# Kernel optimization log

Measured on AMD Instinct MI355X. Metric: run time of the kernel, lower is better.

The kernel has to match this reference:

```python
import jax, jax.numpy as jnp
import numpy as np

NUM_HEADS = 12
LN_EPS = 1e-5
SM_EPS = 1e-6


def layer_norm(x, w, b):
    m = x.mean(-1, keepdims=True)
    v = ((x - m) ** 2).mean(-1, keepdims=True)
    return (x - m) / jnp.sqrt(v + LN_EPS) * w + b


def softmax_with_policy(attn, policy):
    # attn: [B,H,N,N], policy: [B,N,1]
    B, H, N, _ = attn.shape
    attn_policy = policy.reshape(B, 1, 1, N)
    eye = jnp.eye(N, dtype=attn.dtype)[None, None]
    attn_policy = attn_policy + (1.0 - attn_policy) * eye
    m = attn.max(axis=-1, keepdims=True)
    e = jnp.exp(attn - m) * attn_policy
    return (e + SM_EPS / N) / (e.sum(axis=-1, keepdims=True) + SM_EPS)


def create_ys(ncdf, n_ref):
    # ncdf: [B, N-1]; returns ys: [B, n_ref-1]
    B = ncdf.shape[0]
    ys = jnp.linspace(0.0, 1.0, n_ref - 1, dtype=ncdf.dtype)[None, :]
    ys_start = jnp.min(ncdf + (ncdf == 0).astype(ncdf.dtype) * 1e8, axis=1, keepdims=True)
    steps = jnp.arange(n_ref - 1, dtype=ncdf.dtype)[None, :]
    return ys_start + (ys * (n_ref - 2) - ys_start * steps) / (n_ref - 2)


def get_unique_indices(indices, max_value):
    # duplicate indices are replaced by max_value, then re-sorted
    B = indices.shape[0]
    s = jnp.sort(indices, axis=1)
    shifted = jnp.concatenate([s[:, 1:], jnp.ones((B, 1), s.dtype)], axis=1)
    uniq = jnp.where(shifted == s, max_value, s)
    return jnp.sort(uniq, axis=1)


def ats_block(x, policy, norm1_w, norm1_b, qkv_w, proj_w, proj_b,
              norm2_w, norm2_b, fc1_w, fc1_b, fc2_w, fc2_b,
              n_tokens, n_ref_tokens):
    B, N, C = x.shape
    H = NUM_HEADS
    dh = C // H
    scale = dh ** -0.5

    xn = layer_norm(x, norm1_w, norm1_b)
    qkv = (xn @ qkv_w).reshape(B, N, 3, H, dh).transpose(2, 0, 3, 1, 4)  # [3,B,H,N,dh]
    qkv = qkv * policy[None, :, None, :, :]
    q, k, v = qkv[0], qkv[1], qkv[2]

    attn = softmax_with_policy(jnp.einsum('bhnd,bhmd->bhnm', q, k) * scale, policy)

    # --- score assignment ---
    v_norm = jnp.linalg.norm(v.transpose(0, 2, 1, 3).reshape(B, N, C), axis=2)  # [B,N]
    sig = attn[:, :, 0, :].sum(axis=1) * v_norm      # CLS attention row summed over heads
    sig = sig[:, 1:]
    sig = sig / sig.sum(axis=1, keepdims=True)
    order = jnp.argsort(sig, axis=1)                 # ascending
    sorted_scores = jnp.take_along_axis(sig, order, axis=1)

    # --- inverse transform sampling ---
    cdf = jnp.cumsum(sorted_scores, axis=1)
    cmin = cdf.min(axis=1, keepdims=True)
    cmax = cdf.max(axis=1, keepdims=True)
    ncdf = (cdf - cmin) / (cmax - cmin)              # [B, N-1]
    ys = create_ys(ncdf, n_ref_tokens)               # [B, n_ref-1]
    diff = (n_ref_tokens - 1) - (N - 1)
    ncdf_p = jnp.pad(ncdf, ((0, 0), (diff, 0))) if diff > 0 else ncdf
    tokens_to_pick = jnp.argmin(jnp.abs(ys[:, :, None] - ncdf_p[:, None, :]), axis=2) - diff

    uniq = get_unique_indices(tokens_to_pick, N - 1)[:, :N - 1]
    ui = uniq[:, :n_tokens - 1]                      # [B, n_tokens-1]

    # reorder attn rows / raw tokens by significance order, pad a zero row at N-1
    oidx = jnp.broadcast_to(order[:, None, :, None], (B, H, N - 1, N))
    attn_sorted = jnp.take_along_axis(attn[:, :, 1:, :], oidx, axis=2)
    attn_tmp = jnp.pad(attn_sorted, ((0, 0), (0, 0), (0, 1), (0, 0)))
    rx_sorted = jnp.take_along_axis(x[:, 1:, :], jnp.broadcast_to(order[:, :, None], (B, N - 1, C)), axis=1)
    rx_tmp = jnp.pad(rx_sorted, ((0, 0), (0, 1), (0, 0)))

    uidx = jnp.broadcast_to(ui[:, None, :, None], (B, H, n_tokens - 1, N))
    attn_sel = jnp.take_along_axis(attn_tmp, uidx, axis=2)
    rx_sel = jnp.take_along_axis(rx_tmp, jnp.broadcast_to(ui[:, :, None], (B, n_tokens - 1, C)), axis=1)

    attn_new = jnp.concatenate([attn[:, :, 0:1, :], attn_sel], axis=2)     # [B,H,n_tokens,N]
    selected_x = jnp.concatenate([x[:, 0:1, :], rx_sel], axis=1)           # [B,n_tokens,C]
    pol_new = (ui != N - 1).astype(x.dtype)[:, :, None]
    pol_new = jnp.pad(pol_new, ((0, 0), (1, 0), (0, 0)), constant_values=1.0)  # [B,n_tokens,1]

    out = jnp.einsum('bhnm,bhmd->bhnd', attn_new, v)
    out = out.transpose(0, 2, 1, 3).reshape(B, n_tokens, C)
    out = (out @ proj_w + proj_b) * pol_new

    x2 = selected_x + out
    h = jax.nn.gelu(layer_norm(x2, norm2_w, norm2_b) @ fc1_w + fc1_b, approximate=False)
    x2 = x2 + (h @ fc2_w + fc2_b) * pol_new
    return x2, pol_new


def setup_inputs() -> dict:
    key = jax.random.key(0)
    ks = jax.random.split(key, 6)
    B, N, C = 8, 785, 768
    init = lambda k, sh, fan: jax.random.normal(k, sh, jnp.float32) * (fan ** -0.5)
    return {
        'x': jax.random.normal(ks[0], (B, N, C), jnp.float32),
        'policy': jnp.ones((B, N, 1), jnp.float32),
        'norm1_w': jnp.ones((C,), jnp.float32),
        'norm1_b': jnp.zeros((C,), jnp.float32),
        'qkv_w': init(ks[1], (C, 3 * C), C),
        'proj_w': init(ks[2], (C, C), C),
        'proj_b': jnp.zeros((C,), jnp.float32),
        'norm2_w': jnp.ones((C,), jnp.float32),
        'norm2_b': jnp.zeros((C,), jnp.float32),
        'fc1_w': init(ks[3], (C, 4 * C), C),
        'fc1_b': jnp.zeros((4 * C,), jnp.float32),
        'fc2_w': init(ks[4], (4 * C, C), 4 * C),
        'fc2_b': jnp.zeros((C,), jnp.float32),
        'n_tokens': 393,
        'n_ref_tokens': 785,
    }


def reference(x, policy, norm1_w, norm1_b, qkv_w, proj_w, proj_b,
              norm2_w, norm2_b, fc1_w, fc1_b, fc2_w, fc2_b,
              n_tokens, n_ref_tokens):
    return ats_block(x, policy, norm1_w, norm1_b, qkv_w, proj_w, proj_b,
                     norm2_w, norm2_b, fc1_w, fc1_b, fc2_w, fc2_b,
                     int(n_tokens), int(n_ref_tokens))
```

## Files before the change

### kernel.cpp

```cpp
#include <hip/hip_runtime.h>
#include <hip/hip_bf16.h>
#include <float.h>
#include <math.h>
#include <stdint.h>

constexpr int B_   = 8;
constexpr int N_   = 785;
constexpr int C_   = 768;
constexpr int H_   = 12;
constexpr int DH_  = 64;
constexpr int NT_  = 393;
constexpr int QKVC = 3 * C_;
constexpr int BN   = B_ * N_;
constexpr int BT   = B_ * NT_;
constexpr int MSEL = N_ - 1;
constexpr float  SCALE_F = 0.125f;
constexpr double LNEPS   = 1e-5;
constexpr double SMEPS   = 1e-6;

#define DEV static __device__ __forceinline__

typedef __hip_bfloat16 bf16;
typedef __attribute__((ext_vector_type(8))) short frag8;
typedef __attribute__((ext_vector_type(4))) float facc4;

DEV short f2b(float v) { return (short)__hip_bfloat16_raw(__float2bfloat16(v)).x; }
DEV float b2f(short s) {
  union { unsigned int u; float f; } cv;
  cv.u = ((unsigned int)(unsigned short)s) << 16;
  return cv.f;
}

DEV double blockReduceSumD(double v, double* scratch, int nw) {
#pragma unroll
  for (int o = 32; o; o >>= 1) v += __shfl_xor(v, o);
  int lane = threadIdx.x & 63, wid = threadIdx.x >> 6;
  __syncthreads();
  if (lane == 0) scratch[wid] = v;
  __syncthreads();
  double r = scratch[0];
  for (int i = 1; i < nw; i++) r += scratch[i];
  return r;
}
DEV double blockReduceMaxD(double v, double* scratch, int nw) {
#pragma unroll
  for (int o = 32; o; o >>= 1) v = fmax(v, __shfl_xor(v, o));
  int lane = threadIdx.x & 63, wid = threadIdx.x >> 6;
  __syncthreads();
  if (lane == 0) scratch[wid] = v;
  __syncthreads();
  double r = scratch[0];
  for (int i = 1; i < nw; i++) r = fmax(r, scratch[i]);
  return r;
}
DEV float blockReduceSumF(float v, float* scratch, int nw) {
#pragma unroll
  for (int o = 32; o; o >>= 1) v += __shfl_xor(v, o);
  int lane = threadIdx.x & 63, wid = threadIdx.x >> 6;
  __syncthreads();
  if (lane == 0) scratch[wid] = v;
  __syncthreads();
  float r = scratch[0];
  for (int i = 1; i < nw; i++) r += scratch[i];
  return r;
}
DEV float blockReduceMaxF(float v, float* scratch, int nw) {
#pragma unroll
  for (int o = 32; o; o >>= 1) v = fmaxf(v, __shfl_xor(v, o));
  int lane = threadIdx.x & 63, wid = threadIdx.x >> 6;
  __syncthreads();
  if (lane == 0) scratch[wid] = v;
  __syncthreads();
  float r = scratch[0];
  for (int i = 1; i < nw; i++) r = fmaxf(r, scratch[i]);
  return r;
}

__global__ __launch_bounds__(256) void ln1_kernel(
    const float* __restrict__ x, const float* __restrict__ w, const float* __restrict__ b,
    double* __restrict__ xn64, bf16* __restrict__ xnb) {
  int row = blockIdx.x;
  int t = threadIdx.x;
  __shared__ double scr[8];
  const float* xr = x + (size_t)row * C_;
  double vals[3];
#pragma unroll
  for (int i = 0; i < 3; i++) vals[i] = (double)xr[t + i * 256];
  double s = vals[0] + vals[1] + vals[2];
  s = blockReduceSumD(s, scr, 4);
  double mean = s / (double)C_;
  double vs = 0.0;
#pragma unroll
  for (int i = 0; i < 3; i++) { double d = vals[i] - mean; vs += d * d; }
  vs = blockReduceSumD(vs, scr, 4);
  double inv = 1.0 / sqrt(vs / (double)C_ + LNEPS);
#pragma unroll
  for (int i = 0; i < 3; i++) {
    int c = t + i * 256;
    double o = (vals[i] - mean) * inv * (double)w[c] + (double)b[c];
    xn64[(size_t)row * C_ + c] = o;
    xnb[(size_t)row * C_ + c] = __float2bfloat16((float)o);
  }
}

__global__ __launch_bounds__(256) void transpose_bf16(
    const float* __restrict__ W, bf16* __restrict__ Wt, int K, int N) {
  __shared__ float tile[32][33];
  int k0 = blockIdx.y * 32, n0 = blockIdx.x * 32;
  int tx = threadIdx.x & 31, ty = threadIdx.x >> 5;
  for (int i = ty; i < 32; i += 8) {
    int k = k0 + i, n = n0 + tx;
    tile[i][tx] = (k < K && n < N) ? W[(size_t)k * N + n] : 0.f;
  }
  __syncthreads();
  for (int i = ty; i < 32; i += 8) {
    int n = n0 + i, k = k0 + tx;
    if (n < N && k < K) Wt[(size_t)n * K + k] = __float2bfloat16(tile[tx][i]);
  }
}

__global__ __launch_bounds__(256) void gemm_bf16(
    const bf16* __restrict__ A, const bf16* __restrict__ Bt,
    float* __restrict__ Cc, const float* __restrict__ bias,
    const float* __restrict__ rowscale, int M, int K, int Ncols) {
  __shared__ short As[64][40];
  __shared__ short Bs[64][40];
  const short* Ap = (const short*)A;
  const short* Bp = (const short*)Bt;
  int t = threadIdx.x;
  int n0 = blockIdx.x * 64;
  int m0 = blockIdx.y * 64;
  int w = t >> 6, l = t & 63;
  int srow = t >> 2;
  int koff = (t & 3) * 8;
  facc4 acc[4] = {{0, 0, 0, 0}, {0, 0, 0, 0}, {0, 0, 0, 0}, {0, 0, 0, 0}};
  int frow = (l & 15);
  int fk = (l >> 4) * 8;
  for (int k0 = 0; k0 < K; k0 += 32) {
    {
      int4 av = make_int4(0, 0, 0, 0);
      if (m0 + srow < M)
        av = *(const int4*)(Ap + (size_t)(m0 + srow) * K + k0 + koff);
      *(int4*)(&As[srow][koff]) = av;
      int4 bv = *(const int4*)(Bp + (size_t)(n0 + srow) * K + k0 + koff);
      *(int4*)(&Bs[srow][koff]) = bv;
    }
    __syncthreads();
    frag8 a = *(frag8*)(&As[w * 16 + frow][fk]);
#pragma unroll
    for (int nt = 0; nt < 4; nt++) {
      frag8 bfr = *(frag8*)(&Bs[nt * 16 + frow][fk]);
      acc[nt] = __builtin_amdgcn_mfma_f32_16x16x32_bf16(a, bfr, acc[nt], 0, 0, 0);
    }
    __syncthreads();
  }
#pragma unroll
  for (int nt = 0; nt < 4; nt++) {
#pragma unroll
    for (int reg = 0; reg < 4; reg++) {
      int row = m0 + w * 16 + (l >> 4) * 4 + reg;
      int col = n0 + nt * 16 + (l & 15);
      if (row < M) {
        float v = acc[nt][reg];
        if (bias) v += bias[col];
        if (rowscale) v *= rowscale[row];
        Cc[(size_t)row * Ncols + col] = v;
      }
    }
  }
}

__global__ __launch_bounds__(256) void q0_kernel(
    const double* __restrict__ xn64, const float* __restrict__ qkvw,
    const float* __restrict__ policy, double* __restrict__ q064) {
  int b = blockIdx.x;
  int jc = blockIdx.y;
  int t = threadIdx.x;
  int jl = t & 63, ks = t >> 6;
  __shared__ double x0[C_];
  __shared__ double part[4][64];
  for (int i = t; i < C_; i += 256) x0[i] = xn64[(size_t)(b * N_) * C_ + i];
  __syncthreads();
  int j = jc * 64 + jl;
  const float* wp = qkvw + j;
  double a = 0.0;
  int c0 = ks * 192;
#pragma unroll 8
  for (int c = c0; c < c0 + 192; c++) a += x0[c] * (double)wp[(size_t)c * QKVC];
  part[ks][jl] = a;
  __syncthreads();
  if (t < 64) {
    double pol = (double)policy[b * N_];
    q064[b * C_ + jc * 64 + t] =
        (part[0][t] + part[1][t] + part[2][t] + part[3][t]) * pol;
  }
}

__global__ __launch_bounds__(256) void g_kernel(
    const double* __restrict__ q064, const float* __restrict__ qkvw,
    double* __restrict__ g64) {
  int bh = blockIdx.x;
  int b = bh / H_, h = bh % H_;
  int t = threadIdx.x;
  __shared__ double qh[DH_];
  if (t < DH_) qh[t] = q064[b * C_ + h * DH_ + t];
  __syncthreads();
  for (int c = t; c < C_; c += 256) {
    const float* wp = qkvw + (size_t)c * QKVC + C_ + h * DH_;
    double a = 0.0;
#pragma unroll 8
    for (int d = 0; d < DH_; d++) a += qh[d] * (double)wp[d];
    g64[(size_t)bh * C_ + c] = a;
  }
}

__global__ __launch_bounds__(256) void logits_kernel(
    const double* __restrict__ xn64, const double* __restrict__ g64,
    const float* __restrict__ policy, double* __restrict__ l64) {
  int row = blockIdx.x;
  int b = row / N_;
  int n = row % N_;
  int t = threadIdx.x;
  int w = t >> 6, lane = t & 63;
  __shared__ double xr[C_];
  for (int i = t; i < C_; i += 256) xr[i] = xn64[(size_t)row * C_ + i];
  __syncthreads();
  double pol = (double)policy[row];
#pragma unroll
  for (int hh = 0; hh < 3; hh++) {
    int h = w + hh * 4;
    const double* gp = g64 + (size_t)(b * H_ + h) * C_;
    double p = 0.0;
#pragma unroll 4
    for (int i = lane; i < C_; i += 64) p += xr[i] * gp[i];
#pragma unroll
    for (int o = 32; o; o >>= 1) p += __shfl_xor(p, o);
    if (lane == 0) l64[(size_t)(b * H_ + h) * N_ + n] = 0.125 * pol * p;
  }
}

__global__ __launch_bounds__(256) void vnorm_kernel(
    const double* __restrict__ xn64, const float* __restrict__ qkvw,
    const float* __restrict__ policy, double* __restrict__ vnorm2) {
  __shared__ double scr[8];
  int r0 = blockIdx.x * 8;
  int t = threadIdx.x;
  double acc[8][3] = {};
  const double* xb = xn64 + (size_t)r0 * C_;
  for (int c = 0; c < C_; c += 2) {
    const float* wp0 = qkvw + (size_t)c * QKVC + 2 * C_;
    const float* wp1 = wp0 + QKVC;
    double w00 = (double)wp0[t], w01 = (double)wp0[t + 256], w02 = (double)wp0[t + 512];
    double w10 = (double)wp1[t], w11 = (double)wp1[t + 256], w12 = (double)wp1[t + 512];
#pragma unroll
    for (int r = 0; r < 8; r++) {
      double x0 = xb[(size_t)r * C_ + c];
      double x1 = xb[(size_t)r * C_ + c + 1];
      acc[r][0] += x0 * w00; acc[r][1] += x0 * w01; acc[r][2] += x0 * w02;
      acc[r][0] += x1 * w10; acc[r][1] += x1 * w11; acc[r][2] += x1 * w12;
    }
  }
#pragma unroll
  for (int r = 0; r < 8; r++) {
    double p = acc[r][0] * acc[r][0] + acc[r][1] * acc[r][1] + acc[r][2] * acc[r][2];
    double s = blockReduceSumD(p, scr, 4);
    if (t == 0) {
      double pol = (double)policy[r0 + r];
      vnorm2[r0 + r] = s * pol * pol;
    }
  }
}

__global__ __launch_bounds__(256) void softmax0_kernel(
    double* __restrict__ l64, const float* __restrict__ policy) {
  int bh = blockIdx.x;
  int b = bh / H_;
  double* lp = l64 + (size_t)bh * N_;
  __shared__ double scr[8];
  int t = threadIdx.x;
  double mx = -1e300;
  for (int n = t; n < N_; n += 256) mx = fmax(mx, lp[n]);
  mx = blockReduceMaxD(mx, scr, 4);
  double ssum = 0.0;
  for (int n = t; n < N_; n += 256) {
    double pol = (double)policy[b * N_ + n];
    double w = (n == 0) ? 1.0 : pol;
    double e = exp(lp[n] - mx) * w;
    lp[n] = e;
    ssum += e;
  }
  ssum = blockReduceSumD(ssum, scr, 4);
  double denom = ssum + SMEPS;
  double addc = SMEPS / (double)N_;
  for (int n = t; n < N_; n += 256) lp[n] = (lp[n] + addc) / denom;
}

__global__ __launch_bounds__(1024) void select_kernel(
    const double* __restrict__ p0, const double* __restrict__ vnorm2,
    int* __restrict__ selidx, float* __restrict__ poln, float* __restrict__ out_pol) {
  int b = blockIdx.x;
  int t = threadIdx.x;
  __shared__ double sigv[MSEL];
  __shared__ double svals[MSEL];
  __shared__ double nc[MSEL];
  __shared__ int    ord[MSEL];
  __shared__ int    pick[MSEL];
  __shared__ int    spick[MSEL];
  __shared__ int    uq[MSEL];
  __shared__ int    suq[MSEL];
  __shared__ double sh_ys;

  if (t < MSEL) {
    int n = t + 1;
    double s = 0.0;
#pragma unroll
    for (int h = 0; h < H_; h++) s += p0[(size_t)(b * H_ + h) * N_ + n];
    sigv[t] = s * sqrt(vnorm2[b * N_ + n]);
  }
  __syncthreads();
  if (t < MSEL) {
    double v = sigv[t];
    int rank = 0;
    for (int i = 0; i < MSEL; i++) {
      double vi = sigv[i];
      rank += (vi < v) || (vi == v && i < t);
    }
    ord[rank] = t;
    svals[rank] = v;
  }
  __syncthreads();
  if (t == 0) {
    double a = 0.0;
    for (int i = 0; i < MSEL; i++) { a += svals[i]; svals[i] = a; }
  }
  __syncthreads();
  {
    double c0 = svals[0], cN = svals[MSEL - 1];
    if (t < MSEL) nc[t] = (svals[t] - c0) / (cN - c0);
  }
  __syncthreads();
  if (t == 0) {
    double m = 1e300;
    for (int i = 0; i < MSEL; i++) {
      double v = nc[i];
      if (v == 0.0) v += 100000000.0;
      m = fmin(m, v);
    }
    sh_ys = m;
  }
  __syncthreads();
  if (t < MSEL) {
    double s = sh_ys;
    double ysj = (t == MSEL - 1) ? 1.0 : (double)t / 783.0;
    double y = s + (ysj * 783.0 - s * (double)t) / 783.0;
    double bd = 1e300;
    int bi = 0;
    for (int i = 0; i < MSEL; i++) {
      double d = fabs(y - nc[i]);
      if (d < bd) { bd = d; bi = i; }
    }
    pick[t] = bi;
  }
  __syncthreads();
  if (t < MSEL) {
    int p = pick[t];
    int rank = 0;
    for (int i = 0; i < MSEL; i++) {
      int pi = pick[i];
      rank += (pi < p) || (pi == p && i < t);
    }
    spick[rank] = p;
  }
  __syncthreads();
  if (t < MSEL) {
    int s = spick[t];
    int nxt = (t < MSEL - 1) ? spick[t + 1] : 1;
    uq[t] = (nxt == s) ? MSEL : s;
  }
  __syncthreads();
  if (t < MSEL) {
    int u = uq[t];
    int rank = 0;
    for (int i = 0; i < MSEL; i++) {
      int ui = uq[i];
      rank += (ui < u) || (ui == u && i < t);
    }
    suq[rank] = u;
  }
  __syncthreads();
  if (t < NT_) {
    int sel, polI;
    if (t == 0) { sel = 0; polI = 1; }
    else {
      int ut = suq[t - 1];
      polI = (ut != MSEL) ? 1 : 0;
      sel = polI ? (ord[ut] + 1) : -1;
    }
    selidx[b * NT_ + t] = sel;
    poln[b * NT_ + t] = (float)polI;
    out_pol[b * NT_ + t] = (float)polI;
  }
}

__global__ __launch_bounds__(256) void flash_kernel(
    const float* __restrict__ qkv, const int* __restrict__ selidx,
    const float* __restrict__ policy, bf16* __restrict__ attn_bf) {
  int bh = blockIdx.y;
  int b = bh / H_, h = bh % H_;
  int j0 = blockIdx.x * 64;
  int t = threadIdx.x;
  int w = t >> 6, l = t & 63;
  __shared__ short Qs[64][72];
  __shared__ short Ks[64][72];
  __shared__ short Ps[64][72];
  __shared__ short Vs[64][72];
  __shared__ float pol_s[64];
  __shared__ float Vsum[64];

  {
    int jr = t >> 2, d0 = (t & 3) * 16;
    int j = j0 + jr;
    int r = (j < NT_) ? selidx[b * NT_ + j] : -1;
    if (r < 0) r = 0;
    const float* qp = qkv + (size_t)(b * N_ + r) * QKVC + h * DH_ + d0;
#pragma unroll
    for (int i = 0; i < 16; i++) Qs[jr][d0 + i] = f2b(qp[i]);
  }
  if (t < 64) Vsum[t] = 0.f;

  int frow = l & 15, fk = (l >> 4) * 8;
  int base_r = w * 16 + (l >> 4) * 4;
  int coln = l & 15;

  int rrow[4];
#pragma unroll
  for (int r = 0; r < 4; r++) {
    int j = j0 + base_r + r;
    rrow[r] = (j < NT_) ? selidx[b * NT_ + j] : -1;
  }
  float m_run[4] = {-1e30f, -1e30f, -1e30f, -1e30f};
  float s_run[4] = {0.f, 0.f, 0.f, 0.f};
  facc4 Oacc[4] = {{0, 0, 0, 0}, {0, 0, 0, 0}, {0, 0, 0, 0}, {0, 0, 0, 0}};

  for (int n0 = 0; n0 < 832; n0 += 64) {
    {
      int nr = t >> 2, d0 = (t & 3) * 16;
      int n = n0 + nr;
      bool ok = n < N_;
      const float* kp = qkv + (size_t)(b * N_ + (ok ? n : 0)) * QKVC + C_ + h * DH_ + d0;
#pragma unroll
      for (int i = 0; i < 16; i++) Ks[nr][d0 + i] = f2b(ok ? kp[i] : 0.f);
    }
    if (t < 64) {
      int n = n0 + t;
      pol_s[t] = (n < N_) ? policy[b * N_ + n] : 0.f;
    }
    __syncthreads();

    facc4 Sacc[4] = {{0, 0, 0, 0}, {0, 0, 0, 0}, {0, 0, 0, 0}, {0, 0, 0, 0}};
#pragma unroll
    for (int k0 = 0; k0 < 64; k0 += 32) {
      frag8 a = *(frag8*)(&Qs[w * 16 + frow][k0 + fk]);
#pragma unroll
      for (int nt = 0; nt < 4; nt++) {
        frag8 bb = *(frag8*)(&Ks[nt * 16 + frow][k0 + fk]);
        Sacc[nt] = __builtin_amdgcn_mfma_f32_16x16x32_bf16(a, bb, Sacc[nt], 0, 0, 0);
      }
    }
    float S[4][4];
    float tmax[4] = {-1e30f, -1e30f, -1e30f, -1e30f};
#pragma unroll
    for (int nt = 0; nt < 4; nt++) {
#pragma unroll
      for (int r = 0; r < 4; r++) {
        int n = n0 + nt * 16 + coln;
        float v = (n < N_) ? Sacc[nt][r] * SCALE_F : -1e30f;
        S[nt][r] = v;
        tmax[r] = fmaxf(tmax[r], v);
      }
    }
#pragma unroll
    for (int o = 1; o < 16; o <<= 1) {
#pragma unroll
      for (int r = 0; r < 4; r++) tmax[r] = fmaxf(tmax[r], __shfl_xor(tmax[r], o));
    }
    float m_new[4], scl[4], psum[4];
#pragma unroll
    for (int r = 0; r < 4; r++) {
      m_new[r] = fmaxf(m_run[r], tmax[r]);
      scl[r] = expf(m_run[r] - m_new[r]);
      psum[r] = 0.f;
    }
#pragma unroll
    for (int nt = 0; nt < 4; nt++) {
      float pol = pol_s[nt * 16 + coln];
      int n = n0 + nt * 16 + coln;
#pragma unroll
      for (int r = 0; r < 4; r++) {
        float wgt = (n == rrow[r]) ? 1.f : pol;
        float e = expf(S[nt][r] - m_new[r]) * wgt;
        S[nt][r] = e;
        psum[r] += e;
      }
    }
#pragma unroll
    for (int o = 1; o < 16; o <<= 1) {
#pragma unroll
      for (int r = 0; r < 4; r++) psum[r] += __shfl_xor(psum[r], o);
    }
#pragma unroll
    for (int r = 0; r < 4; r++) {
      s_run[r] = s_run[r] * scl[r] + psum[r];
      m_run[r] = m_new[r];
    }
    __syncthreads();

#pragma unroll
    for (int nt = 0; nt < 4; nt++) {
#pragma unroll
      for (int r = 0; r < 4; r++) Ps[base_r + r][nt * 16 + coln] = f2b(S[nt][r]);
    }
    {
      int nr = t >> 2, d0 = (t & 3) * 16;
      int n = n0 + nr;
      bool ok = n < N_;
      const float* vp = qkv + (size_t)(b * N_ + (ok ? n : 0)) * QKVC + 2 * C_ + h * DH_ + d0;
#pragma unroll
      for (int i = 0; i < 16; i++) Vs[d0 + i][nr] = f2b(ok ? vp[i] : 0.f);
    }
    __syncthreads();

    if (t < 64) {
      float a = 0.f;
#pragma unroll 16
      for (int k = 0; k < 64; k++) a += b2f(Vs[t][k]);
      Vsum[t] += a;
    }
#pragma unroll
    for (int dt = 0; dt < 4; dt++) {
#pragma unroll
      for (int r = 0; r < 4; r++) Oacc[dt][r] *= scl[r];
    }
#pragma unroll
    for (int k0 = 0; k0 < 64; k0 += 32) {
      frag8 a = *(frag8*)(&Ps[w * 16 + frow][k0 + fk]);
#pragma unroll
      for (int dt = 0; dt < 4; dt++) {
        frag8 bb = *(frag8*)(&Vs[dt * 16 + frow][k0 + fk]);
        Oacc[dt] = __builtin_amdgcn_mfma_f32_16x16x32_bf16(a, bb, Oacc[dt], 0, 0, 0);
      }
    }
  }
  __syncthreads();
  float addc = 1e-6f / (float)N_;
#pragma unroll
  for (int r = 0; r < 4; r++) {
    int j = j0 + base_r + r;
    if (j >= NT_) continue;
    float denom = s_run[r] + 1e-6f;
#pragma unroll
    for (int dt = 0; dt < 4; dt++) {
      int d = dt * 16 + coln;
      float val = (Oacc[dt][r] + addc * Vsum[d]) / denom;
      attn_bf[(size_t)(b * NT_ + j) * C_ + h * DH_ + d] = __float2bfloat16(val);
    }
  }
}

__global__ __launch_bounds__(256) void e2_kernel(
    const float* __restrict__ cbuf, const float* __restrict__ poln,
    const int* __restrict__ selidx, const float* __restrict__ x, float* __restrict__ x2) {
  int row = blockIdx.x;
  int t = threadIdx.x;
  int b = row / NT_;
  int r = selidx[row];
  float pn = poln[row];
  for (int i = t; i < C_; i += 256) {
    float sx = (r >= 0) ? x[(size_t)(b * N_ + r) * C_ + i] : 0.f;
    x2[(size_t)row * C_ + i] = sx + cbuf[(size_t)row * C_ + i] * pn;
  }
}

__global__ __launch_bounds__(256) void ln2_kernel(
    const float* __restrict__ xin, const float* __restrict__ w, const float* __restrict__ b,
    bf16* __restrict__ xoutb) {
  int row = blockIdx.x;
  int t = threadIdx.x;
  __shared__ float scr[8];
  const float* xr = xin + (size_t)row * C_;
  float vals[3];
#pragma unroll
  for (int i = 0; i < 3; i++) vals[i] = xr[t + i * 256];
  float s = vals[0] + vals[1] + vals[2];
  s = blockReduceSumF(s, scr, 4);
  float mean = s / (float)C_;
  float vs = 0.f;
#pragma unroll
  for (int i = 0; i < 3; i++) { float d = vals[i] - mean; vs += d * d; }
  vs = blockReduceSumF(vs, scr, 4);
  float sd = sqrtf(vs / (float)C_ + 1e-5f);
#pragma unroll
  for (int i = 0; i < 3; i++) {
    int c = t + i * 256;
    xoutb[(size_t)row * C_ + c] =
        __float2bfloat16((vals[i] - mean) / sd * w[c] + b[c]);
  }
}

DEV float gelu_exact(float v) { return 0.5f * v * (1.0f + erff(v * 0.70710678118654752f)); }

__global__ __launch_bounds__(256) void gelu_kernel(
    const float* __restrict__ h, bf16* __restrict__ hb) {
  size_t i = (size_t)blockIdx.x * 256 + threadIdx.x;
  float4 v = ((const float4*)h)[i];
  ushort4 o;
  o.x = __hip_bfloat16_raw(__float2bfloat16(gelu_exact(v.x))).x;
  o.y = __hip_bfloat16_raw(__float2bfloat16(gelu_exact(v.y))).x;
  o.z = __hip_bfloat16_raw(__float2bfloat16(gelu_exact(v.z))).x;
  o.w = __hip_bfloat16_raw(__float2bfloat16(gelu_exact(v.w))).x;
  ((ushort4*)hb)[i] = o;
}

__global__ __launch_bounds__(256) void e4_kernel(
    const float* __restrict__ x2, const float* __restrict__ cbuf,
    const float* __restrict__ poln, float* __restrict__ out) {
  int row = blockIdx.x;
  int t = threadIdx.x;
  float pn = poln[row];
  for (int i = t; i < C_; i += 256) {
    float v = x2[(size_t)row * C_ + i] + cbuf[(size_t)row * C_ + i] * pn;
    out[(size_t)row * C_ + i] = v;
  }
}

extern "C" void kernel_launch(void* const* d_in, const int* in_sizes, int n_in,
                              void* d_out, int out_size, void* d_ws, size_t ws_size,
                              hipStream_t stream) {
  const float* x      = (const float*)d_in[0];
  const float* policy = (const float*)d_in[1];
  const float* n1w    = (const float*)d_in[2];
  const float* n1b    = (const float*)d_in[3];
  const float* qkvw   = (const float*)d_in[4];
  const float* projw  = (const float*)d_in[5];
  const float* projb  = (const float*)d_in[6];
  const float* n2w    = (const float*)d_in[7];
  const float* n2b    = (const float*)d_in[8];
  const float* fc1w   = (const float*)d_in[9];
  const float* fc1b   = (const float*)d_in[10];
  const float* fc2w   = (const float*)d_in[11];
  const float* fc2b   = (const float*)d_in[12];

  char* ws = (char*)d_ws;
  size_t off = 0;
  auto alloc = [&](size_t bytes) {
    size_t o = off;
    off += (bytes + 255) & ~(size_t)255;
    return o;
  };

  double* xn64    = (double*)(ws + alloc((size_t)BN * C_ * 8));
  bf16*   xnb     = (bf16*)(ws + alloc((size_t)BN * C_ * 2));
  float*  qkv32   = (float*)(ws + alloc((size_t)BN * QKVC * 4));
  double* vnorm2  = (double*)(ws + alloc((size_t)BN * 8));
  double* q064    = (double*)(ws + alloc((size_t)B_ * C_ * 8));
  double* g64     = (double*)(ws + alloc((size_t)B_ * H_ * C_ * 8));
  double* l64     = (double*)(ws + alloc((size_t)B_ * H_ * N_ * 8));
  int*    selidx  = (int*)(ws + alloc((size_t)BT * 4));
  float*  poln    = (float*)(ws + alloc((size_t)BT * 4));
  bf16*   attn_bf = (bf16*)(ws + alloc((size_t)BT * C_ * 2));
  float*  cbuf    = (float*)(ws + alloc((size_t)BT * C_ * 4));
  float*  x2      = (float*)(ws + alloc((size_t)BT * C_ * 4));
  bf16*   qkvw_t  = (bf16*)(ws + alloc((size_t)QKVC * C_ * 2));
  bf16*   projw_t = (bf16*)(ws + alloc((size_t)C_ * C_ * 2));
  bf16*   fc1w_t  = (bf16*)(ws + alloc((size_t)4 * C_ * C_ * 2));
  bf16*   fc2w_t  = (bf16*)(ws + alloc((size_t)C_ * 4 * C_ * 2));
  bf16*   xn2b    = (bf16*)(ws + alloc((size_t)BT * C_ * 2));
  float*  h32     = (float*)(ws + alloc((size_t)BT * 4 * C_ * 4));
  bf16*   h_bf    = (bf16*)(ws + alloc((size_t)BT * 4 * C_ * 2));
  if (off > ws_size) return;

  float* out_x = (float*)d_out;
  float* out_p = out_x + (size_t)BT * C_;

  transpose_bf16<<<dim3(QKVC / 32, C_ / 32), 256, 0, stream>>>(qkvw, qkvw_t, C_, QKVC);
  transpose_bf16<<<dim3(C_ / 32, C_ / 32), 256, 0, stream>>>(projw, projw_t, C_, C_);
  transpose_bf16<<<dim3(4 * C_ / 32, C_ / 32), 256, 0, stream>>>(fc1w, fc1w_t, C_, 4 * C_);
  transpose_bf16<<<dim3(C_ / 32, 4 * C_ / 32), 256, 0, stream>>>(fc2w, fc2w_t, 4 * C_, C_);

  ln1_kernel<<<BN, 256, 0, stream>>>(x, n1w, n1b, xn64, xnb);

  {
    dim3 g(QKVC / 64, (BN + 63) / 64);
    gemm_bf16<<<g, 256, 0, stream>>>(xnb, qkvw_t, qkv32, nullptr, policy, BN, C_, QKVC);
  }

  q0_kernel<<<dim3(B_, C_ / 64), 256, 0, stream>>>(xn64, qkvw, policy, q064);
  g_kernel<<<B_ * H_, 256, 0, stream>>>(q064, qkvw, g64);
  logits_kernel<<<BN, 256, 0, stream>>>(xn64, g64, policy, l64);
  vnorm_kernel<<<BN / 8, 256, 0, stream>>>(xn64, qkvw, policy, vnorm2);
  softmax0_kernel<<<B_ * H_, 256, 0, stream>>>(l64, policy);
  select_kernel<<<B_, 1024, 0, stream>>>(l64, vnorm2, selidx, poln, out_p);

  {
    dim3 g((NT_ + 63) / 64, B_ * H_);
    flash_kernel<<<g, 256, 0, stream>>>(qkv32, selidx, policy, attn_bf);
  }

  {
    dim3 g(C_ / 64, (BT + 63) / 64);
    gemm_bf16<<<g, 256, 0, stream>>>(attn_bf, projw_t, cbuf, projb, nullptr, BT, C_, C_);
  }
  e2_kernel<<<BT, 256, 0, stream>>>(cbuf, poln, selidx, x, x2);
  ln2_kernel<<<BT, 256, 0, stream>>>(x2, n2w, n2b, xn2b);
  {
    dim3 g(4 * C_ / 64, (BT + 63) / 64);
    gemm_bf16<<<g, 256, 0, stream>>>(xn2b, fc1w_t, h32, fc1b, nullptr, BT, C_, 4 * C_);
  }
  gelu_kernel<<<(BT * 4 * C_) / 1024, 256, 0, stream>>>(h32, h_bf);
  {
    dim3 g(C_ / 64, (BT + 63) / 64);
    gemm_bf16<<<g, 256, 0, stream>>>(h_bf, fc2w_t, cbuf, fc2b, nullptr, BT, 4 * C_, C_);
  }
  e4_kernel<<<BT, 256, 0, stream>>>(x2, cbuf, poln, out_x);
}
```

Before: 892.6 us.

## Use 128x128 GEMM tiles with 4x4 MFMA per wave and fuse GELU into fc1

```diff
diff --git a/kernel.cpp b/kernel.cpp
--- a/kernel.cpp
+++ b/kernel.cpp
@@ -30,6 +30,7 @@
   cv.u = ((unsigned int)(unsigned short)s) << 16;
   return cv.f;
 }
+DEV float gelu_exact(float v) { return 0.5f * v * (1.0f + erff(v * 0.70710678118654752f)); }
 
 DEV double blockReduceSumD(double v, double* scratch, int nw) {
 #pragma unroll
@@ -119,52 +120,69 @@
   }
 }
 
-__global__ __launch_bounds__(256) void gemm_bf16(
+__global__ __launch_bounds__(256) void gemm128(
     const bf16* __restrict__ A, const bf16* __restrict__ Bt,
     float* __restrict__ Cc, const float* __restrict__ bias,
-    const float* __restrict__ rowscale, int M, int K, int Ncols) {
-  __shared__ short As[64][40];
-  __shared__ short Bs[64][40];
+    const float* __restrict__ rowscale, int M, int K, int Ncols,
+    bf16* __restrict__ gelu_bf) {
+  __shared__ short As[128][40];
+  __shared__ short Bs[128][40];
   const short* Ap = (const short*)A;
   const short* Bp = (const short*)Bt;
   int t = threadIdx.x;
-  int n0 = blockIdx.x * 64;
-  int m0 = blockIdx.y * 64;
+  int n0 = blockIdx.x * 128;
+  int m0 = blockIdx.y * 128;
   int w = t >> 6, l = t & 63;
-  int srow = t >> 2;
-  int koff = (t & 3) * 8;
-  facc4 acc[4] = {{0, 0, 0, 0}, {0, 0, 0, 0}, {0, 0, 0, 0}, {0, 0, 0, 0}};
-  int frow = (l & 15);
-  int fk = (l >> 4) * 8;
+  int wr = w >> 1, wc = w & 1;
+  int srow = t >> 1;
+  int koff = (t & 1) * 16;
+  int fr = l & 15, fk = (l >> 4) * 8;
+  facc4 acc[4][4] = {};
   for (int k0 = 0; k0 < K; k0 += 32) {
-    {
-      int4 av = make_int4(0, 0, 0, 0);
-      if (m0 + srow < M)
-        av = *(const int4*)(Ap + (size_t)(m0 + srow) * K + k0 + koff);
-      *(int4*)(&As[srow][koff]) = av;
-      int4 bv = *(const int4*)(Bp + (size_t)(n0 + srow) * K + k0 + koff);
-      *(int4*)(&Bs[srow][koff]) = bv;
-    }
+    int4 av0 = make_int4(0, 0, 0, 0), av1 = make_int4(0, 0, 0, 0);
+    if (m0 + srow < M) {
+      const short* ap = Ap + (size_t)(m0 + srow) * K + k0 + koff;
+      av0 = *(const int4*)ap;
+      av1 = *(const int4*)(ap + 8);
+    }
+    const short* bp = Bp + (size_t)(n0 + srow) * K + k0 + koff;
+    int4 bv0 = *(const int4*)bp;
+    int4 bv1 = *(const int4*)(bp + 8);
+    *(int4*)(&As[srow][koff])     = av0;
+    *(int4*)(&As[srow][koff + 8]) = av1;
+    *(int4*)(&Bs[srow][koff])     = bv0;
+    *(int4*)(&Bs[srow][koff + 8]) = bv1;
     __syncthreads();
-    frag8 a = *(frag8*)(&As[w * 16 + frow][fk]);
-#pragma unroll
-    for (int nt = 0; nt < 4; nt++) {
-      frag8 bfr = *(frag8*)(&Bs[nt * 16 + frow][fk]);
-      acc[nt] = __builtin_amdgcn_mfma_f32_16x16x32_bf16(a, bfr, acc[nt], 0, 0, 0);
-    }
+    frag8 af[4], bf[4];
+#pragma unroll
+    for (int i = 0; i < 4; i++) af[i] = *(frag8*)(&As[wr * 64 + i * 16 + fr][fk]);
+#pragma unroll
+    for (int j = 0; j < 4; j++) bf[j] = *(frag8*)(&Bs[wc * 64 + j * 16 + fr][fk]);
+#pragma unroll
+    for (int i = 0; i < 4; i++)
+#pragma unroll
+      for (int j = 0; j < 4; j++)
+        acc[i][j] = __builtin_amdgcn_mfma_f32_16x16x32_bf16(af[i], bf[j], acc[i][j], 0, 0, 0);
     __syncthreads();
   }
 #pragma unroll
-  for (int nt = 0; nt < 4; nt++) {
+  for (int i = 0; i < 4; i++) {
 #pragma unroll
     for (int reg = 0; reg < 4; reg++) {
-      int row = m0 + w * 16 + (l >> 4) * 4 + reg;
-      int col = n0 + nt * 16 + (l & 15);
-      if (row < M) {
-        float v = acc[nt][reg];
+      int row = m0 + wr * 64 + i * 16 + (l >> 4) * 4 + reg;
+      if (row >= M) continue;
+      float rs = rowscale ? rowscale[row] : 1.f;
+#pragma unroll
+      for (int j = 0; j < 4; j++) {
+        int col = n0 + wc * 64 + j * 16 + fr;
+        float v = acc[i][j][reg];
         if (bias) v += bias[col];
-        if (rowscale) v *= rowscale[row];
-        Cc[(size_t)row * Ncols + col] = v;
+        if (gelu_bf) {
+          gelu_bf[(size_t)row * Ncols + col] = __float2bfloat16(gelu_exact(v));
+        } else {
+          v *= rs;
+          Cc[(size_t)row * Ncols + col] = v;
+        }
       }
     }
   }
@@ -605,20 +623,6 @@
     xoutb[(size_t)row * C_ + c] =
         __float2bfloat16((vals[i] - mean) / sd * w[c] + b[c]);
   }
-}
-
-DEV float gelu_exact(float v) { return 0.5f * v * (1.0f + erff(v * 0.70710678118654752f)); }
-
-__global__ __launch_bounds__(256) void gelu_kernel(
-    const float* __restrict__ h, bf16* __restrict__ hb) {
-  size_t i = (size_t)blockIdx.x * 256 + threadIdx.x;
-  float4 v = ((const float4*)h)[i];
-  ushort4 o;
-  o.x = __hip_bfloat16_raw(__float2bfloat16(gelu_exact(v.x))).x;
-  o.y = __hip_bfloat16_raw(__float2bfloat16(gelu_exact(v.y))).x;
-  o.z = __hip_bfloat16_raw(__float2bfloat16(gelu_exact(v.z))).x;
-  o.w = __hip_bfloat16_raw(__float2bfloat16(gelu_exact(v.w))).x;
-  ((ushort4*)hb)[i] = o;
 }
 
 __global__ __launch_bounds__(256) void e4_kernel(
@@ -675,7 +679,6 @@
   bf16*   fc1w_t  = (bf16*)(ws + alloc((size_t)4 * C_ * C_ * 2));
   bf16*   fc2w_t  = (bf16*)(ws + alloc((size_t)C_ * 4 * C_ * 2));
   bf16*   xn2b    = (bf16*)(ws + alloc((size_t)BT * C_ * 2));
-  float*  h32     = (float*)(ws + alloc((size_t)BT * 4 * C_ * 4));
   bf16*   h_bf    = (bf16*)(ws + alloc((size_t)BT * 4 * C_ * 2));
   if (off > ws_size) return;
 
@@ -690,8 +693,8 @@
   ln1_kernel<<<BN, 256, 0, stream>>>(x, n1w, n1b, xn64, xnb);
 
   {
-    dim3 g(QKVC / 64, (BN + 63) / 64);
-    gemm_bf16<<<g, 256, 0, stream>>>(xnb, qkvw_t, qkv32, nullptr, policy, BN, C_, QKVC);
+    dim3 g(QKVC / 128, (BN + 127) / 128);
+    gemm128<<<g, 256, 0, stream>>>(xnb, qkvw_t, qkv32, nullptr, policy, BN, C_, QKVC, nullptr);
   }
 
   q0_kernel<<<dim3(B_, C_ / 64), 256, 0, stream>>>(xn64, qkvw, policy, q064);
@@ -707,19 +710,18 @@
   }
 
   {
-    dim3 g(C_ / 64, (BT + 63) / 64);
-    gemm_bf16<<<g, 256, 0, stream>>>(attn_bf, projw_t, cbuf, projb, nullptr, BT, C_, C_);
+    dim3 g(C_ / 128, (BT + 127) / 128);
+    gemm128<<<g, 256, 0, stream>>>(attn_bf, projw_t, cbuf, projb, nullptr, BT, C_, C_, nullptr);
   }
   e2_kernel<<<BT, 256, 0, stream>>>(cbuf, poln, selidx, x, x2);
   ln2_kernel<<<BT, 256, 0, stream>>>(x2, n2w, n2b, xn2b);
   {
-    dim3 g(4 * C_ / 64, (BT + 63) / 64);
-    gemm_bf16<<<g, 256, 0, stream>>>(xn2b, fc1w_t, h32, fc1b, nullptr, BT, C_, 4 * C_);
-  }
-  gelu_kernel<<<(BT * 4 * C_) / 1024, 256, 0, stream>>>(h32, h_bf);
+    dim3 g(4 * C_ / 128, (BT + 127) / 128);
+    gemm128<<<g, 256, 0, stream>>>(xn2b, fc1w_t, nullptr, fc1b, nullptr, BT, C_, 4 * C_, h_bf);
+  }
   {
-    dim3 g(C_ / 64, (BT + 63) / 64);
-    gemm_bf16<<<g, 256, 0, stream>>>(h_bf, fc2w_t, cbuf, fc2b, nullptr, BT, 4 * C_, C_);
+    dim3 g(C_ / 128, (BT + 127) / 128);
+    gemm128<<<g, 256, 0, stream>>>(h_bf, fc2w_t, cbuf, fc2b, nullptr, BT, 4 * C_, C_, nullptr);
   }
   e4_kernel<<<BT, 256, 0, stream>>>(x2, cbuf, poln, out_x);
 }
```

Result: slower. 923.5 us (+3.5%).
